# Performance work log

Measured on AMD Instinct MI355X. Metric: run time of the kernel, lower is better.

The kernel has to match this reference:

```python
import jax, jax.numpy as jnp
import numpy as np
from jax import lax

SD = 16  # sample_duration
POOL_KS = (SD, SD * 3 // 4, SD // 2, SD // 4)  # (16, 12, 8, 4)


def conv3d_same(x, w, b):
    # x: [B,C,T,H,W], w: [O,I,3,3,3]
    y = lax.conv_general_dilated(
        x, w, window_strides=(1, 1, 1), padding=[(1, 1), (1, 1), (1, 1)],
        dimension_numbers=("NCDHW", "OIDHW", "NCDHW"))
    return y + b[None, :, None, None, None]


def maxpool_t(x, k):
    # MaxPool3d((k,1,1), stride=1): max over sliding temporal window
    return lax.reduce_window(x, -jnp.inf, lax.max,
                             (1, 1, k, 1, 1), (1, 1, 1, 1, 1), "VALID")


def head1x1(x, w, b):
    # 1x1x1 Conv3d as einsum; x: [B,C,T,H,W], w: [O,C]
    return jnp.einsum("bcthw,oc->bothw", x, w) + b[None, :, None, None, None]


def cls_prob(score):
    # _RPN.reshape(x,2) -> softmax(dim=1) -> reshape back to [B,30,T,H,W]
    B, C, T, H, W = score.shape
    s2 = score.reshape(B, 2, (C * T) // 2, H, W)
    p = jax.nn.softmax(s2, axis=1)
    return p.reshape(B, C, T, H, W)


def setup_inputs() -> dict:
    key = jax.random.key(0)
    ks = jax.random.split(key, 12)
    din, B, H, W = 512, 2, 28, 28
    s = 0.05
    return {
        "base_feat": jax.random.normal(ks[0], (B, din, SD, H, W), jnp.float32),
        "im_info": jnp.ones((B, 3), jnp.float32) * 448.0,
        "gt_boxes": jax.random.uniform(ks[1], (B, 20, 5), jnp.float32),
        "gt_rois": jax.random.uniform(ks[2], (B, 20, SD, 5), jnp.float32),
        "W_conv": jax.random.normal(ks[3], (din, din, 3, 3, 3), jnp.float32) * 0.01,
        "b_conv": jnp.zeros((din,), jnp.float32),
        "W_cls": jax.random.normal(ks[4], (30, din), jnp.float32) * s,
        "b_cls": jnp.zeros((30,), jnp.float32),
        "W_bbox": jax.random.normal(ks[5], (960, din), jnp.float32) * s,
        "b_bbox": jnp.zeros((960,), jnp.float32),
        "W_bbox_34": jax.random.normal(ks[6], (720, din), jnp.float32) * s,
        "b_bbox_34": jnp.zeros((720,), jnp.float32),
        "W_bbox_2": jax.random.normal(ks[7], (480, din), jnp.float32) * s,
        "b_bbox_2": jnp.zeros((480,), jnp.float32),
        "W_bbox_4": jax.random.normal(ks[8], (240, din), jnp.float32) * s,
        "b_bbox_4": jnp.zeros((240,), jnp.float32),
    }


def reference(base_feat, im_info, gt_boxes, gt_rois,
              W_conv, b_conv, W_cls, b_cls,
              W_bbox, b_bbox, W_bbox_34, b_bbox_34,
              W_bbox_2, b_bbox_2, W_bbox_4, b_bbox_4):
    # RPN conv + relu
    x = jax.nn.relu(conv3d_same(base_feat, W_conv, b_conv))
    # four temporal max-pool branches (T' = 1, 5, 9, 13)
    pools = [maxpool_t(x, k) for k in POOL_KS]
    # NOTE: original code applies the SAME RPN_cls_score conv to all branches
    probs = tuple(cls_prob(head1x1(p, W_cls, b_cls)) for p in pools)
    bbox_ws = [(W_bbox, b_bbox), (W_bbox_34, b_bbox_34),
               (W_bbox_2, b_bbox_2), (W_bbox_4, b_bbox_4)]
    bboxes = tuple(head1x1(p, w, b) for p, (w, b) in zip(pools, bbox_ws))
    return probs + bboxes
```

## Files before the change

kernel.cpp:

```cpp
#include <hip/hip_runtime.h>

typedef unsigned short u16;
typedef unsigned int   u32;
typedef __bf16  bf16x8 __attribute__((ext_vector_type(8)));
typedef float   f32x4  __attribute__((ext_vector_type(4)));

__device__ __forceinline__ float bf2f(u16 u) {
    u32 v = ((u32)u) << 16;
    return __builtin_bit_cast(float, v);
}
__device__ __forceinline__ u16 f2bf(float f) {
    u32 u = __builtin_bit_cast(u32, f);
    return (u16)((u + 0x7FFFu + ((u >> 16) & 1u)) >> 16);
}
__device__ __forceinline__ float ldf(const void* p, long i, int f32) {
    return f32 ? ((const float*)p)[i] : bf2f(((const u16*)p)[i]);
}
__device__ __forceinline__ void gl2lds16(const u16* g, u16* l) {
    __builtin_amdgcn_global_load_lds(
        (const __attribute__((address_space(1))) void*)g,
        (__attribute__((address_space(3))) void*)l, 16, 0, 0);
}

__global__ void detect_dtype(const u32* __restrict__ im, int* __restrict__ flag)
{
    if (blockIdx.x == 0 && threadIdx.x == 0)
        *flag = (im[0] == 0x43E00000u) ? 1 : 0;
}

__global__ void zero_kernel(uint4* __restrict__ p, const int n)
{
    int i = blockIdx.x * 256 + threadIdx.x;
    if (i < n) p[i] = uint4{0u, 0u, 0u, 0u};
}

__global__ void pad_fill(const void* __restrict__ src, u16* __restrict__ xpad,
                         const int* __restrict__ flag)
{
    const int f32 = *flag;
    __shared__ u16 lds[56 * 40];
    int blk = blockIdx.x;
    const int h2  = blk % 14;  blk /= 14;
    const int c32 = blk & 15;  blk >>= 4;
    const int t   = blk & 15;
    const int b   = blk >> 4;
    const int tid = threadIdx.x;
    const long sbase = ((long)(b * 512 + c32 * 32) * 16 + t) * 784 + h2 * 56;
    #pragma unroll
    for (int it = tid; it < 1792; it += 256) {
        const int c = it / 56, p = it - c * 56;
        float v = f32 ? ((const float*)src)[sbase + (long)c * 12544 + p]
                      : bf2f(((const u16*)src)[sbase + (long)c * 12544 + p]);
        lds[p * 40 + c] = f2bf(v);
    }
    __syncthreads();
    if (tid < 224) {
        const int p = tid >> 2, g = tid & 3;
        const int h = h2 * 2 + p / 28, w = p % 28;
        const long o = (((long)(b * 18 + t + 1) * 30 + h + 1) * 30 + (w + 1)) * 512
                       + c32 * 32 + g * 8;
        *(uint4*)&xpad[o] = *(const uint4*)&lds[p * 40 + g * 8];
    }
}

__global__ void wt_transform(const void* __restrict__ wconv, u16* __restrict__ wt,
                             const int* __restrict__ flag)
{
    const int f32 = *flag;
    __shared__ u16 lds[256 * 28];
    const int tid = threadIdx.x;
    const int pair_base = blockIdx.x * 256;
    const long s0 = (long)pair_base * 27;
    for (int it = tid; it < 256 * 27; it += 256) {
        const int p = it / 27, o = it - p * 27;
        float v = f32 ? ((const float*)wconv)[s0 + it]
                      : bf2f(((const u16*)wconv)[s0 + it]);
        lds[p * 28 + o] = f2bf(v);
    }
    __syncthreads();
    #pragma unroll
    for (int off = 0; off < 27; ++off)
        wt[(long)off * 262144 + pair_base + tid] = lds[tid * 28 + off];
}

__global__ void cvt_heads(const void* s0, const void* s1, const void* s2,
                          const void* s3, const void* s4,
                          u16* __restrict__ dst, const int* __restrict__ flag)
{
    const int f32 = *flag;
    int i = blockIdx.x * 256 + threadIdx.x;
    if (i >= 1244160) return;
    const void* s; long j;
    if      (i < 15360)   { s = s0; j = i; }
    else if (i < 506880)  { s = s1; j = i - 15360; }
    else if (i < 875520)  { s = s2; j = i - 506880; }
    else if (i < 1121280) { s = s3; j = i - 875520; }
    else                  { s = s4; j = i - 1121280; }
    dst[i] = f2bf(ldf(s, j, f32));
}

__global__ void cvt_bias(const void* s0, const void* s1, const void* s2,
                         const void* s3, const void* s4, const void* s5,
                         float* __restrict__ dst, const int* __restrict__ flag)
{
    const int f32 = *flag;
    int i = blockIdx.x * 256 + threadIdx.x;
    if (i >= 2942) return;
    float v;
    if      (i < 512)  v = ldf(s0, i, f32);
    else if (i < 542)  v = ldf(s1, i - 512, f32);
    else if (i < 1502) v = ldf(s2, i - 542, f32);
    else if (i < 2222) v = ldf(s3, i - 1502, f32);
    else if (i < 2702) v = ldf(s4, i - 2222, f32);
    else               v = ldf(s5, i - 2702, f32);
    dst[i] = v;
}

__global__ __launch_bounds__(512, 2) void conv_gemm256(
    const u16* __restrict__ xpad, const u16* __restrict__ wt,
    const float* __restrict__ bfs, u16* __restrict__ y)
{
    __shared__ u16 smem[65536];
    const int tid = threadIdx.x;

    const int bx  = blockIdx.x;
    const int xcd = bx & 7, pos = bx >> 3;
    const int L   = (xcd < 4 ? xcd * 25 : 100 + (xcd - 4) * 24) + pos;
    const int m_base = (L & 1) * 256;
    const int n_base = (L >> 1) * 256;

    const int rq  = tid >> 2;
    const int gsw = (((tid & 3) ^ ((tid >> 3) & 3))) * 8;
    const u16* pa0 = wt + (long)(m_base + rq) * 512 + gsw;
    const u16* pa1 = pa0 + 128 * 512;

    const int n0 = n_base + rq;
    const int n1 = n0 + 128;
    int b0 = n0 / 12544, r0 = n0 % 12544;
    int t0 = r0 / 784,   q0 = r0 % 784;
    int h0 = q0 / 28,    w0 = q0 % 28;
    int b1 = n1 / 12544, r1 = n1 % 12544;
    int t1 = r1 / 784,   q1 = r1 % 784;
    int h1 = q1 / 28,    w1 = q1 % 28;
    const int sa0 = ((b0 * 18 + t0) * 30 + h0) * 30 + w0;
    const int sa1 = ((b1 * 18 + t1) * 30 + h1) * 30 + w1;
    const u16* pb0 = xpad + (long)sa0 * 512 + gsw;
    const u16* pb1 = xpad + (long)sa1 * 512 + gsw;

    const int lane = tid & 63, wid = tid >> 6;
    const int l16 = lane & 15, quad = lane >> 4;
    const int wm = wid >> 2;
    const int wn = wid & 3;
    const int slot  = (quad ^ ((l16 >> 1) & 3)) * 8;
    const int aoffs = (wm * 128 + l16) * 32 + slot;
    const int boffs = 8192 + (wn * 64 + l16) * 32 + slot;

    f32x4 acc[8][4] = {};

    #pragma unroll
    for (int k = 0; k < 3; ++k) {
        u16* dst = smem + (k << 14);
        gl2lds16(pa0 + k * 32, dst + tid * 8);
        gl2lds16(pa1 + k * 32, dst + 4096  + tid * 8);
        gl2lds16(pb0 + k * 32, dst + 8192  + tid * 8);
        gl2lds16(pb1 + k * 32, dst + 12288 + tid * 8);
    }

#define KTILE(ktl, STG, GATE)                                                  \
    {                                                                          \
        asm volatile("s_waitcnt vmcnt(" #GATE ")" ::: "memory");               \
        asm volatile("s_barrier" ::: "memory");                                \
        const u16* buf = smem + (((ktl) & 3) << 14);                           \
        bf16x8 af[8], bfr[4];                                                  \
        _Pragma("unroll")                                                      \
        for (int mi = 0; mi < 4; ++mi)                                         \
            af[mi] = *(const bf16x8*)&buf[aoffs + mi * 512];                   \
        _Pragma("unroll")                                                      \
        for (int ni = 0; ni < 4; ++ni)                                         \
            bfr[ni] = *(const bf16x8*)&buf[boffs + ni * 512];                  \
        _Pragma("unroll")                                                      \
        for (int mi = 4; mi < 8; ++mi)                                         \
            af[mi] = *(const bf16x8*)&buf[aoffs + mi * 512];                   \
        if (STG) {                                                             \
            const int kts = (ktl) + 3;                                         \
            const int tap = kts >> 4, kc = kts & 15;                           \
            const int kd = tap / 9, r9 = tap - kd * 9;                         \
            const int kh = r9 / 3,  kw = r9 - kh * 3;                          \
            const long aoff = (long)tap * 262144 + kc * 32;                    \
            const long boff = (long)(kd * 900 + kh * 30 + kw) * 512 + kc * 32; \
            u16* dst = smem + ((kts & 3) << 14);                               \
            gl2lds16(pa0 + aoff, dst + tid * 8);                               \
            gl2lds16(pa1 + aoff, dst + 4096  + tid * 8);                       \
            gl2lds16(pb0 + boff, dst + 8192  + tid * 8);                       \
            gl2lds16(pb1 + boff, dst + 12288 + tid * 8);                       \
        }                                                                      \
        __builtin_amdgcn_s_setprio(1);                                         \
        _Pragma("unroll")                                                      \
        for (int mi = 0; mi < 4; ++mi)                                         \
            _Pragma("unroll")                                                  \
            for (int ni = 0; ni < 4; ++ni)                                     \
                acc[mi][ni] = __builtin_amdgcn_mfma_f32_16x16x32_bf16(         \
                    af[mi], bfr[ni], acc[mi][ni], 0, 0, 0);                    \
        _Pragma("unroll")                                                      \
        for (int mi = 4; mi < 8; ++mi)                                         \
            _Pragma("unroll")                                                  \
            for (int ni = 0; ni < 4; ++ni)                                     \
                acc[mi][ni] = __builtin_amdgcn_mfma_f32_16x16x32_bf16(         \
                    af[mi], bfr[ni], acc[mi][ni], 0, 0, 0);                    \
        __builtin_amdgcn_s_setprio(0);                                         \
    }

    for (int kt = 0; kt < 429; ++kt) KTILE(kt, 1, 8)
    KTILE(429, 0, 8)
    KTILE(430, 0, 4)
    KTILE(431, 0, 0)
#undef KTILE

    #pragma unroll
    for (int mi = 0; mi < 8; ++mi) {
        const int mrow = m_base + wm * 128 + mi * 16 + quad * 4;
        float bias[4];
        #pragma unroll
        for (int r = 0; r < 4; ++r) bias[r] = bfs[mrow + r];
        #pragma unroll
        for (int ni = 0; ni < 4; ++ni) {
            const int ng = n_base + wn * 64 + ni * 16 + l16;
            f32x4 a = acc[mi][ni];
            u16 o0 = f2bf(fmaxf(a[0] + bias[0], 0.f));
            u16 o1 = f2bf(fmaxf(a[1] + bias[1], 0.f));
            u16 o2 = f2bf(fmaxf(a[2] + bias[2], 0.f));
            u16 o3 = f2bf(fmaxf(a[3] + bias[3], 0.f));
            uint2 pv;
            pv.x = (u32)o0 | ((u32)o1 << 16);
            pv.y = (u32)o2 | ((u32)o3 << 16);
            *(uint2*)&y[(long)ng * 512 + mrow] = pv;
        }
    }
}

__device__ __forceinline__ uint4 max8(uint4 A, uint4 Bv)
{
    const u16* a = (const u16*)&A;
    const u16* b = (const u16*)&Bv;
    uint4 R;
    u16* r = (u16*)&R;
    #pragma unroll
    for (int i = 0; i < 8; ++i) r[i] = (bf2f(a[i]) >= bf2f(b[i])) ? a[i] : b[i];
    return R;
}

__global__ void pool4_kernel(const u16* __restrict__ y, u16* __restrict__ p4)
{
    int g = blockIdx.x * 256 + threadIdx.x;
    if (g >= 2 * 13 * 784 * 64) return;
    const int c8 = g & 63;
    int pos = g >> 6;
    const int hw = pos % 784; pos /= 784;
    const int t0 = pos % 13; const int b = pos / 13;
    const u16* src = y + ((long)((b * 16 + t0) * 784 + hw)) * 512 + c8 * 8;
    uint4 v0 = *(const uint4*)(src);
    uint4 v1 = *(const uint4*)(src + 401408);
    uint4 v2 = *(const uint4*)(src + 802816);
    uint4 v3 = *(const uint4*)(src + 1204224);
    uint4 m = max8(max8(v0, v1), max8(v2, v3));
    *(uint4*)&p4[((long)((b * 13 + t0) * 784 + hw)) * 512 + c8 * 8] = m;
}

__global__ void pools2(const u16* __restrict__ p4, u16* __restrict__ p8,
                       u16* __restrict__ p12, u16* __restrict__ p16)
{
    int g = blockIdx.x * 256 + threadIdx.x;
    if (g >= 1505280) return;
    int Td; u16* dst; int nwin;
    if (g < 903168)       { Td = 9; dst = p8;  nwin = 2; }
    else if (g < 1404928) { g -= 903168;  Td = 5; dst = p12; nwin = 3; }
    else                  { g -= 1404928; Td = 1; dst = p16; nwin = 4; }
    const int c8 = g & 63;
    int pos = g >> 6;
    const int hw = pos % 784; pos /= 784;
    const int t = pos % Td; const int b = pos / Td;
    const u16* src = p4 + ((long)((b * 13 + t) * 784 + hw)) * 512 + c8 * 8;
    uint4 m = *(const uint4*)(src);
    #pragma unroll 3
    for (int j = 1; j < nwin; ++j)
        m = max8(m, *(const uint4*)(src + (long)j * 4 * 784 * 512));
    *(uint4*)&dst[((long)((b * Td + t) * 784 + hw)) * 512 + c8 * 8] = m;
}

__global__ __launch_bounds__(256, 2) void heads_gemm(
    const u16* __restrict__ p16, const u16* __restrict__ p12,
    const u16* __restrict__ p8,  const u16* __restrict__ p4,
    const u16* __restrict__ wcls, const u16* __restrict__ wb1,
    const u16* __restrict__ wb34, const u16* __restrict__ wb2,
    const u16* __restrict__ wb4,  const float* __restrict__ bfs,
    float* __restrict__ clsr, void* __restrict__ outv,
    const int* __restrict__ flag)
{
    const int f32 = *flag;
    int bid = blockIdx.x;
    const u16* pool; const u16* wbp; int Ti, CH, nt, mt; long boff, coff, ooff;
    if (bid < 104)      {             nt = bid % 13;  mt = bid / 13;  pool = p16; wbp = wb1;  Ti = 1;  CH = 960; boff = 542;  coff = 0;      ooff = 1317120; }
    else if (bid < 476) { bid -= 104; nt = bid % 62;  mt = bid / 62;  pool = p12; wbp = wb34; Ti = 5;  CH = 720; boff = 1502; coff = 47040;  ooff = 2822400; }
    else if (bid < 920) { bid -= 476; nt = bid % 111; mt = bid / 111; pool = p8;  wbp = wb2;  Ti = 9;  CH = 480; boff = 2222; coff = 282240; ooff = 8467200; }
    else                { bid -= 920; nt = bid % 160; mt = bid / 160; pool = p4;  wbp = wb4;  Ti = 13; CH = 240; boff = 2702; coff = 705600; ooff = 15240960; }
    const int M = 30 + CH;
    const int THW = Ti * 784;
    const int N = 2 * THW;
    const int n_base = nt * 128;
    const int m_base = mt * 128;

    __shared__ u16 lds_a[128 * 64];
    __shared__ u16 lds_b[128 * 64];
    const int tid = threadIdx.x;
    const int lane = tid & 63;
    const int wid  = tid >> 6;
    const int quad = lane >> 4;
    const int l16  = lane & 15;
    const int wm = (wid & 1) * 64;
    const int wn = (wid >> 1) * 64;
    const int srow = tid >> 3;
    const int lc8  = ((tid & 7) ^ (srow & 7)) * 8;

    const u16* arow[4]; const u16* brow[4];
    #pragma unroll
    for (int j = 0; j < 4; ++j) {
        int m = m_base + j * 32 + srow; if (m > M - 1) m = M - 1;
        arow[j] = ((m < 30) ? (wcls + m * 512) : (wbp + (m - 30) * 512)) + lc8;
        int n = n_base + j * 32 + srow; if (n > N - 1) n = N - 1;
        brow[j] = pool + (long)n * 512 + lc8;
    }

    u16* ldst_a = &lds_a[tid * 8];
    u16* ldst_b = &lds_b[tid * 8];

    int rowA[4], rowB[4];
    #pragma unroll
    for (int i = 0; i < 4; ++i) {
        rowA[i] = (wm + i * 16 + l16) * 64;
        rowB[i] = (wn + i * 16 + l16) * 64;
    }
    const int cx  = l16 & 7;
    const int ch0 = (quad ^ cx) * 8;
    const int ch1 = ((4 + quad) ^ cx) * 8;

    f32x4 acc[4][4] = {};
    for (int kc = 0; kc < 8; ++kc) {
        const int kcol = kc * 64;
        #pragma unroll
        for (int j = 0; j < 4; ++j)
            gl2lds16(arow[j] + kcol, ldst_a + j * 2048);
        #pragma unroll
        for (int j = 0; j < 4; ++j)
            gl2lds16(brow[j] + kcol, ldst_b + j * 2048);
        __syncthreads();
        #pragma unroll
        for (int h = 0; h < 2; ++h) {
            const int co = h ? ch1 : ch0;
            bf16x8 af[4], bfr[4];
            #pragma unroll
            for (int mi = 0; mi < 4; ++mi)
                af[mi]  = *(const bf16x8*)&lds_a[rowA[mi] + co];
            #pragma unroll
            for (int ni = 0; ni < 4; ++ni)
                bfr[ni] = *(const bf16x8*)&lds_b[rowB[ni] + co];
            #pragma unroll
            for (int mi = 0; mi < 4; ++mi)
                #pragma unroll
                for (int ni = 0; ni < 4; ++ni)
                    acc[mi][ni] = __builtin_amdgcn_mfma_f32_16x16x32_bf16(
                        af[mi], bfr[ni], acc[mi][ni], 0, 0, 0);
        }
        __syncthreads();
    }
    const float* bcls = bfs + 512;
    const float* bb   = bfs + boff;
    #pragma unroll
    for (int mi = 0; mi < 4; ++mi) {
        const int mrow = m_base + wm + mi * 16 + quad * 4;
        #pragma unroll
        for (int ni = 0; ni < 4; ++ni) {
            const int ng = n_base + wn + ni * 16 + l16;
            if (ng >= N) continue;
            const int b  = ng / THW;
            const int rr = ng % THW;
            f32x4 a = acc[mi][ni];
            #pragma unroll
            for (int r = 0; r < 4; ++r) {
                const int m = mrow + r;
                if (m >= M) break;
                const float bias = (m < 30) ? bcls[m] : bb[m - 30];
                const float v = a[r] + bias;
                if (m < 30) {
                    clsr[coff + ((long)(b * 30 + m)) * THW + rr] = v;
                } else {
                    const long oi = ooff + ((long)(b * CH + (m - 30))) * THW + rr;
                    if (f32) ((float*)outv)[oi] = v;
                    else     ((u16*)outv)[oi]   = f2bf(v);
                }
            }
        }
    }
}

__global__ void softmax_all(const float* __restrict__ clsr,
                            void* __restrict__ outv, const int* __restrict__ flag)
{
    const int f32 = *flag;
    int g = blockIdx.x * 256 + threadIdx.x;
    if (g >= 658560) return;
    int Ti; long off;
    if      (g < 23520)  { Ti = 1;  off = 0; }
    else if (g < 141120) { Ti = 5;  off = 47040;  g -= 23520; }
    else if (g < 352800) { Ti = 9;  off = 282240; g -= 141120; }
    else                 { Ti = 13; off = 705600; g -= 352800; }
    const int THW = Ti * 784;
    const int rr = g % THW;
    int r2 = g / THW;
    const int j = r2 % 15; const int b = r2 / 15;
    const long i0 = off + ((long)(b * 30 + j)) * THW + rr;
    const long i1 = off + ((long)(b * 30 + j + 15)) * THW + rr;
    const float s0 = clsr[i0], s1 = clsr[i1];
    const float mx = fmaxf(s0, s1);
    const float e0 = __expf(s0 - mx), e1 = __expf(s1 - mx);
    const float inv = 1.0f / (e0 + e1);
    if (f32) {
        ((float*)outv)[i0] = e0 * inv;
        ((float*)outv)[i1] = e1 * inv;
    } else {
        ((u16*)outv)[i0] = f2bf(e0 * inv);
        ((u16*)outv)[i1] = f2bf(e1 * inv);
    }
}

extern "C" void kernel_launch(void* const* d_in, const int* in_sizes, int n_in,
                              void* d_out, int out_size, void* d_ws, size_t ws_size,
                              hipStream_t stream)
{
    const void* base_feat = d_in[0];
    const u32*  im_info   = (const u32*)d_in[1];
    const void* W_conv    = d_in[4];
    const void* b_conv    = d_in[5];
    const void* W_cls     = d_in[6];
    const void* b_cls     = d_in[7];
    const void* W_bbox    = d_in[8];
    const void* b_bbox    = d_in[9];
    const void* W_bbox34  = d_in[10];
    const void* b_bbox34  = d_in[11];
    const void* W_bbox2   = d_in[12];
    const void* b_bbox2   = d_in[13];
    const void* W_bbox4   = d_in[14];
    const void* b_bbox4   = d_in[15];

    char* ws = (char*)d_ws;
    u16*   xpad = (u16*)  (ws + 0);
    u16*   wt   = (u16*)  (ws + 33177600);
    u16*   y    = (u16*)  (ws + 47333376);
    u16*   p4   = (u16*)  (ws + 73023488);
    u16*   p8   = (u16*)  (ws + 93896704);
    u16*   p12  = (u16*)  (ws + 108347392);
    u16*   p16  = (u16*)  (ws + 116375552);
    float* clsr = (float*)(ws + 117981184);
    int*   flag = (int*)  (ws + 123249664);
    u16*   whd  = (u16*)  (ws + 123249728);
    float* bfs  = (float*)(ws + 125738048);

    u16* w_cls_b  = whd;
    u16* w_b1_b   = whd + 15360;
    u16* w_b34_b  = whd + 506880;
    u16* w_b2_b   = whd + 875520;
    u16* w_b4_b   = whd + 1121280;

    detect_dtype<<<1, 64, 0, stream>>>(im_info, flag);
    zero_kernel<<<8100, 256, 0, stream>>>((uint4*)xpad, 2073600);
    pad_fill<<<7168, 256, 0, stream>>>(base_feat, xpad, flag);
    wt_transform<<<1024, 256, 0, stream>>>(W_conv, wt, flag);
    cvt_heads<<<4860, 256, 0, stream>>>(W_cls, W_bbox, W_bbox34, W_bbox2, W_bbox4,
                                        whd, flag);
    cvt_bias<<<12, 256, 0, stream>>>(b_conv, b_cls, b_bbox, b_bbox34, b_bbox2,
                                     b_bbox4, bfs, flag);

    conv_gemm256<<<196, 512, 0, stream>>>(xpad, wt, bfs, y);

    pool4_kernel<<<5096, 256, 0, stream>>>(y, p4);
    pools2<<<5880, 256, 0, stream>>>(p4, p8, p12, p16);

    heads_gemm<<<1400, 256, 0, stream>>>(p16, p12, p8, p4,
                                         w_cls_b, w_b1_b, w_b34_b, w_b2_b, w_b4_b,
                                         bfs, clsr, d_out, flag);

    softmax_all<<<2573, 256, 0, stream>>>(clsr, d_out, flag);
}
```

Measured before the change: 582.4 us.

## Fuse pooling kernels, double-buffer heads GEMM, inline dtype detection, merge converters

The two temporal max-pool kernels become one kernel in which each thread loads all 16 time steps once and builds every window size from shared partial maxima (pairs, quads, then 8/12/16). This removes the round trip through p4. The heads GEMM now uses a double-buffered LDS pipeline that prefetches the next K chunk while MFMAs run, with raised wave priority. The dtype flag kernel is replaced by an inline check of im_info in each kernel, and the weight and bias conversion kernels are merged to cut launch count. The fused pool kernel launches only 392 blocks and holds many registers per thread, which may reduce occupancy and memory parallelism.

```diff
diff --git a/kernel.cpp b/kernel.cpp
--- a/kernel.cpp
+++ b/kernel.cpp
@@ -16,18 +16,15 @@
 __device__ __forceinline__ float ldf(const void* p, long i, int f32) {
     return f32 ? ((const float*)p)[i] : bf2f(((const u16*)p)[i]);
 }
+__device__ __forceinline__ int is_f32(const u32* im) {
+    return im[0] == 0x43E00000u;
+}
 __device__ __forceinline__ void gl2lds16(const u16* g, u16* l) {
     __builtin_amdgcn_global_load_lds(
         (const __attribute__((address_space(1))) void*)g,
         (__attribute__((address_space(3))) void*)l, 16, 0, 0);
 }
 
-__global__ void detect_dtype(const u32* __restrict__ im, int* __restrict__ flag)
-{
-    if (blockIdx.x == 0 && threadIdx.x == 0)
-        *flag = (im[0] == 0x43E00000u) ? 1 : 0;
-}
-
 __global__ void zero_kernel(uint4* __restrict__ p, const int n)
 {
     int i = blockIdx.x * 256 + threadIdx.x;
@@ -35,9 +32,9 @@
 }
 
 __global__ void pad_fill(const void* __restrict__ src, u16* __restrict__ xpad,
-                         const int* __restrict__ flag)
-{
-    const int f32 = *flag;
+                         const u32* __restrict__ im)
+{
+    const int f32 = is_f32(im);
     __shared__ u16 lds[56 * 40];
     int blk = blockIdx.x;
     const int h2  = blk % 14;  blk /= 14;
@@ -64,9 +61,9 @@
 }
 
 __global__ void wt_transform(const void* __restrict__ wconv, u16* __restrict__ wt,
-                             const int* __restrict__ flag)
-{
-    const int f32 = *flag;
+                             const u32* __restrict__ im)
+{
+    const int f32 = is_f32(im);
     __shared__ u16 lds[256 * 28];
     const int tid = threadIdx.x;
     const int pair_base = blockIdx.x * 256;
@@ -83,37 +80,35 @@
         wt[(long)off * 262144 + pair_base + tid] = lds[tid * 28 + off];
 }
 
-__global__ void cvt_heads(const void* s0, const void* s1, const void* s2,
-                          const void* s3, const void* s4,
-                          u16* __restrict__ dst, const int* __restrict__ flag)
-{
-    const int f32 = *flag;
+__global__ void cvt_all(const void* s0, const void* s1, const void* s2,
+                        const void* s3, const void* s4,
+                        const void* b0, const void* b1, const void* b2,
+                        const void* b3, const void* b4, const void* b5,
+                        u16* __restrict__ whd, float* __restrict__ bfs,
+                        const u32* __restrict__ im)
+{
+    const int f32 = is_f32(im);
     int i = blockIdx.x * 256 + threadIdx.x;
-    if (i >= 1244160) return;
-    const void* s; long j;
-    if      (i < 15360)   { s = s0; j = i; }
-    else if (i < 506880)  { s = s1; j = i - 15360; }
-    else if (i < 875520)  { s = s2; j = i - 506880; }
-    else if (i < 1121280) { s = s3; j = i - 875520; }
-    else                  { s = s4; j = i - 1121280; }
-    dst[i] = f2bf(ldf(s, j, f32));
-}
-
-__global__ void cvt_bias(const void* s0, const void* s1, const void* s2,
-                         const void* s3, const void* s4, const void* s5,
-                         float* __restrict__ dst, const int* __restrict__ flag)
-{
-    const int f32 = *flag;
-    int i = blockIdx.x * 256 + threadIdx.x;
+    if (i < 1244160) {
+        const void* s; long j;
+        if      (i < 15360)   { s = s0; j = i; }
+        else if (i < 506880)  { s = s1; j = i - 15360; }
+        else if (i < 875520)  { s = s2; j = i - 506880; }
+        else if (i < 1121280) { s = s3; j = i - 875520; }
+        else                  { s = s4; j = i - 1121280; }
+        whd[i] = f2bf(ldf(s, j, f32));
+        return;
+    }
+    i -= 1244160;
     if (i >= 2942) return;
     float v;
-    if      (i < 512)  v = ldf(s0, i, f32);
-    else if (i < 542)  v = ldf(s1, i - 512, f32);
-    else if (i < 1502) v = ldf(s2, i - 542, f32);
-    else if (i < 2222) v = ldf(s3, i - 1502, f32);
-    else if (i < 2702) v = ldf(s4, i - 2222, f32);
-    else               v = ldf(s5, i - 2702, f32);
-    dst[i] = v;
+    if      (i < 512)  v = ldf(b0, i, f32);
+    else if (i < 542)  v = ldf(b1, i - 512, f32);
+    else if (i < 1502) v = ldf(b2, i - 542, f32);
+    else if (i < 2222) v = ldf(b3, i - 1502, f32);
+    else if (i < 2702) v = ldf(b4, i - 2222, f32);
+    else               v = ldf(b5, i - 2702, f32);
+    bfs[i] = v;
 }
 
 __global__ __launch_bounds__(512, 2) void conv_gemm256(
@@ -249,42 +244,45 @@
     return R;
 }
 
-__global__ void pool4_kernel(const u16* __restrict__ y, u16* __restrict__ p4)
+__global__ void pool_all(const u16* __restrict__ y, u16* __restrict__ p4,
+                         u16* __restrict__ p8, u16* __restrict__ p12,
+                         u16* __restrict__ p16)
 {
     int g = blockIdx.x * 256 + threadIdx.x;
-    if (g >= 2 * 13 * 784 * 64) return;
+    if (g >= 100352) return;
     const int c8 = g & 63;
     int pos = g >> 6;
-    const int hw = pos % 784; pos /= 784;
-    const int t0 = pos % 13; const int b = pos / 13;
-    const u16* src = y + ((long)((b * 16 + t0) * 784 + hw)) * 512 + c8 * 8;
-    uint4 v0 = *(const uint4*)(src);
-    uint4 v1 = *(const uint4*)(src + 401408);
-    uint4 v2 = *(const uint4*)(src + 802816);
-    uint4 v3 = *(const uint4*)(src + 1204224);
-    uint4 m = max8(max8(v0, v1), max8(v2, v3));
-    *(uint4*)&p4[((long)((b * 13 + t0) * 784 + hw)) * 512 + c8 * 8] = m;
-}
-
-__global__ void pools2(const u16* __restrict__ p4, u16* __restrict__ p8,
-                       u16* __restrict__ p12, u16* __restrict__ p16)
-{
-    int g = blockIdx.x * 256 + threadIdx.x;
-    if (g >= 1505280) return;
-    int Td; u16* dst; int nwin;
-    if (g < 903168)       { Td = 9; dst = p8;  nwin = 2; }
-    else if (g < 1404928) { g -= 903168;  Td = 5; dst = p12; nwin = 3; }
-    else                  { g -= 1404928; Td = 1; dst = p16; nwin = 4; }
-    const int c8 = g & 63;
-    int pos = g >> 6;
-    const int hw = pos % 784; pos /= 784;
-    const int t = pos % Td; const int b = pos / Td;
-    const u16* src = p4 + ((long)((b * 13 + t) * 784 + hw)) * 512 + c8 * 8;
-    uint4 m = *(const uint4*)(src);
-    #pragma unroll 3
-    for (int j = 1; j < nwin; ++j)
-        m = max8(m, *(const uint4*)(src + (long)j * 4 * 784 * 512));
-    *(uint4*)&dst[((long)((b * Td + t) * 784 + hw)) * 512 + c8 * 8] = m;
+    const int hw = pos % 784; const int b = pos / 784;
+    const u16* src = y + ((long)(b * 16) * 784 + hw) * 512 + c8 * 8;
+    uint4 v[16];
+    #pragma unroll
+    for (int t = 0; t < 16; ++t)
+        v[t] = *(const uint4*)(src + (long)t * 401408);
+    uint4 pr[15];
+    #pragma unroll
+    for (int t = 0; t < 15; ++t) pr[t] = max8(v[t], v[t + 1]);
+    uint4 qd[13];
+    #pragma unroll
+    for (int t = 0; t < 13; ++t) qd[t] = max8(pr[t], pr[t + 2]);
+    uint4 e8[9];
+    #pragma unroll
+    for (int t = 0; t < 9; ++t) e8[t] = max8(qd[t], qd[t + 4]);
+    uint4 e12[5];
+    #pragma unroll
+    for (int t = 0; t < 5; ++t) e12[t] = max8(e8[t], qd[t + 8]);
+    uint4 e16 = max8(e8[0], e8[8]);
+
+    const long col = (long)hw * 512 + c8 * 8;
+    #pragma unroll
+    for (int t = 0; t < 13; ++t)
+        *(uint4*)&p4[((long)(b * 13 + t) * 784) * 512 + col] = qd[t];
+    #pragma unroll
+    for (int t = 0; t < 9; ++t)
+        *(uint4*)&p8[((long)(b * 9 + t) * 784) * 512 + col] = e8[t];
+    #pragma unroll
+    for (int t = 0; t < 5; ++t)
+        *(uint4*)&p12[((long)(b * 5 + t) * 784) * 512 + col] = e12[t];
+    *(uint4*)&p16[((long)b * 784) * 512 + col] = e16;
 }
 
 __global__ __launch_bounds__(256, 2) void heads_gemm(
@@ -294,9 +292,9 @@
     const u16* __restrict__ wb34, const u16* __restrict__ wb2,
     const u16* __restrict__ wb4,  const float* __restrict__ bfs,
     float* __restrict__ clsr, void* __restrict__ outv,
-    const int* __restrict__ flag)
-{
-    const int f32 = *flag;
+    const u32* __restrict__ im)
+{
+    const int f32 = is_f32(im);
     int bid = blockIdx.x;
     const u16* pool; const u16* wbp; int Ti, CH, nt, mt; long boff, coff, ooff;
     if (bid < 104)      {             nt = bid % 13;  mt = bid / 13;  pool = p16; wbp = wb1;  Ti = 1;  CH = 960; boff = 542;  coff = 0;      ooff = 1317120; }
@@ -309,8 +307,7 @@
     const int n_base = nt * 128;
     const int m_base = mt * 128;
 
-    __shared__ u16 lds_a[128 * 64];
-    __shared__ u16 lds_b[128 * 64];
+    __shared__ u16 lds[32768];
     const int tid = threadIdx.x;
     const int lane = tid & 63;
     const int wid  = tid >> 6;
@@ -330,48 +327,65 @@
         brow[j] = pool + (long)n * 512 + lc8;
     }
 
-    u16* ldst_a = &lds_a[tid * 8];
-    u16* ldst_b = &lds_b[tid * 8];
-
     int rowA[4], rowB[4];
     #pragma unroll
     for (int i = 0; i < 4; ++i) {
         rowA[i] = (wm + i * 16 + l16) * 64;
-        rowB[i] = (wn + i * 16 + l16) * 64;
+        rowB[i] = 8192 + (wn + i * 16 + l16) * 64;
     }
     const int cx  = l16 & 7;
     const int ch0 = (quad ^ cx) * 8;
     const int ch1 = ((4 + quad) ^ cx) * 8;
 
+    #pragma unroll
+    for (int j = 0; j < 4; ++j)
+        gl2lds16(arow[j], &lds[tid * 8 + j * 2048]);
+    #pragma unroll
+    for (int j = 0; j < 4; ++j)
+        gl2lds16(brow[j], &lds[8192 + tid * 8 + j * 2048]);
+
     f32x4 acc[4][4] = {};
     for (int kc = 0; kc < 8; ++kc) {
-        const int kcol = kc * 64;
-        #pragma unroll
-        for (int j = 0; j < 4; ++j)
-            gl2lds16(arow[j] + kcol, ldst_a + j * 2048);
-        #pragma unroll
-        for (int j = 0; j < 4; ++j)
-            gl2lds16(brow[j] + kcol, ldst_b + j * 2048);
-        __syncthreads();
-        #pragma unroll
-        for (int h = 0; h < 2; ++h) {
-            const int co = h ? ch1 : ch0;
-            bf16x8 af[4], bfr[4];
+        asm volatile("s_waitcnt vmcnt(0)" ::: "memory");
+        asm volatile("s_barrier" ::: "memory");
+        const u16* buf = lds + (kc & 1) * 16384;
+        bf16x8 af[8], bfr[8];
+        #pragma unroll
+        for (int mi = 0; mi < 4; ++mi) {
+            af[mi]     = *(const bf16x8*)&buf[rowA[mi] + ch0];
+            af[mi + 4] = *(const bf16x8*)&buf[rowA[mi] + ch1];
+        }
+        #pragma unroll
+        for (int ni = 0; ni < 4; ++ni) {
+            bfr[ni]     = *(const bf16x8*)&buf[rowB[ni] + ch0];
+            bfr[ni + 4] = *(const bf16x8*)&buf[rowB[ni] + ch1];
+        }
+        if (kc < 7) {
+            u16* dst = lds + ((kc + 1) & 1) * 16384 + tid * 8;
+            const int kcol = (kc + 1) * 64;
             #pragma unroll
-            for (int mi = 0; mi < 4; ++mi)
-                af[mi]  = *(const bf16x8*)&lds_a[rowA[mi] + co];
+            for (int j = 0; j < 4; ++j)
+                gl2lds16(arow[j] + kcol, dst + j * 2048);
+            #pragma unroll
+            for (int j = 0; j < 4; ++j)
+                gl2lds16(brow[j] + kcol, dst + 8192 + j * 2048);
+        }
+        __builtin_amdgcn_s_setprio(1);
+        #pragma unroll
+        for (int mi = 0; mi < 4; ++mi)
             #pragma unroll
             for (int ni = 0; ni < 4; ++ni)
-                bfr[ni] = *(const bf16x8*)&lds_b[rowB[ni] + co];
+                acc[mi][ni] = __builtin_amdgcn_mfma_f32_16x16x32_bf16(
+                    af[mi], bfr[ni], acc[mi][ni], 0, 0, 0);
+        #pragma unroll
+        for (int mi = 0; mi < 4; ++mi)
             #pragma unroll
-            for (int mi = 0; mi < 4; ++mi)
-                #pragma unroll
-                for (int ni = 0; ni < 4; ++ni)
-                    acc[mi][ni] = __builtin_amdgcn_mfma_f32_16x16x32_bf16(
-                        af[mi], bfr[ni], acc[mi][ni], 0, 0, 0);
-        }
-        __syncthreads();
-    }
+            for (int ni = 0; ni < 4; ++ni)
+                acc[mi][ni] = __builtin_amdgcn_mfma_f32_16x16x32_bf16(
+                    af[mi + 4], bfr[ni + 4], acc[mi][ni], 0, 0, 0);
+        __builtin_amdgcn_s_setprio(0);
+    }
+
     const float* bcls = bfs + 512;
     const float* bb   = bfs + boff;
     #pragma unroll
@@ -403,9 +417,9 @@
 }
 
 __global__ void softmax_all(const float* __restrict__ clsr,
-                            void* __restrict__ outv, const int* __restrict__ flag)
-{
-    const int f32 = *flag;
+                            void* __restrict__ outv, const u32* __restrict__ im)
+{
+    const int f32 = is_f32(im);
     int g = blockIdx.x * 256 + threadIdx.x;
     if (g >= 658560) return;
     int Ti; long off;
@@ -460,7 +474,6 @@
     u16*   p12  = (u16*)  (ws + 108347392);
     u16*   p16  = (u16*)  (ws + 116375552);
     float* clsr = (float*)(ws + 117981184);
-    int*   flag = (int*)  (ws + 123249664);
     u16*   whd  = (u16*)  (ws + 123249728);
     float* bfs  = (float*)(ws + 125738048);
 
@@ -470,23 +483,20 @@
     u16* w_b2_b   = whd + 875520;
     u16* w_b4_b   = whd + 1121280;
 
-    detect_dtype<<<1, 64, 0, stream>>>(im_info, flag);
     zero_kernel<<<8100, 256, 0, stream>>>((uint4*)xpad, 2073600);
-    pad_fill<<<7168, 256, 0, stream>>>(base_feat, xpad, flag);
-    wt_transform<<<1024, 256, 0, stream>>>(W_conv, wt, flag);
-    cvt_heads<<<4860, 256, 0, stream>>>(W_cls, W_bbox, W_bbox34, W_bbox2, W_bbox4,
-                                        whd, flag);
-    cvt_bias<<<12, 256, 0, stream>>>(b_conv, b_cls, b_bbox, b_bbox34, b_bbox2,
-                                     b_bbox4, bfs, flag);
+    pad_fill<<<7168, 256, 0, stream>>>(base_feat, xpad, im_info);
+    wt_transform<<<1024, 256, 0, stream>>>(W_conv, wt, im_info);
+    cvt_all<<<4873, 256, 0, stream>>>(W_cls, W_bbox, W_bbox34, W_bbox2, W_bbox4,
+                                      b_conv, b_cls, b_bbox, b_bbox34, b_bbox2,
+                                      b_bbox4, whd, bfs, im_info);
 
     conv_gemm256<<<196, 512, 0, stream>>>(xpad, wt, bfs, y);
 
-    pool4_kernel<<<5096, 256, 0, stream>>>(y, p4);
-    pools2<<<5880, 256, 0, stream>>>(p4, p8, p12, p16);
+    pool_all<<<392, 256, 0, stream>>>(y, p4, p8, p12, p16);
 
     heads_gemm<<<1400, 256, 0, stream>>>(p16, p12, p8, p4,
                                          w_cls_b, w_b1_b, w_b34_b, w_b2_b, w_b4_b,
-                                         bfs, clsr, d_out, flag);
-
-    softmax_all<<<2573, 256, 0, stream>>>(clsr, d_out, flag);
-}
+                                         bfs, clsr, d_out, im_info);
+
+    softmax_all<<<2573, 256, 0, stream>>>(clsr, d_out, im_info);
+}
```

Result: slower. 622.5 us (+6.9%).
